# Kernel optimization log

Hardware: AMD Instinct MI355X
Metric: run time of the kernel (lower is better)

The kernel has to match this reference:

```python
import jax, jax.numpy as jnp
import numpy as np
from jax import lax

NUM_GROUPS = 16
EPS = 1e-5
POOL = 4
CLAMP_MIN, CLAMP_MAX = 0.0, 1.0


def setup_inputs() -> dict:
    key = jax.random.key(0)
    k = jax.random.split(key, 6)
    x = jax.random.normal(k[0], (128, 8, 128, 128), dtype=jnp.float32)
    conv_w = jax.random.normal(k[1], (64, 8, 3, 3), dtype=jnp.float32) * 0.1
    conv_b = jax.random.normal(k[2], (64,), dtype=jnp.float32) * 0.1
    gn_w = jnp.ones((64,), dtype=jnp.float32) + 0.1 * jax.random.normal(k[3], (64,), dtype=jnp.float32)
    gn_b = 0.1 * jax.random.normal(k[4], (64,), dtype=jnp.float32)
    scale = jnp.ones((64, 1, 1), dtype=jnp.float32) + 0.1 * jax.random.normal(k[5], (64, 1, 1), dtype=jnp.float32)
    return {"x": x, "conv_w": conv_w, "conv_b": conv_b, "gn_w": gn_w, "gn_b": gn_b, "scale": scale}


def reference(x, conv_w, conv_b, gn_w, gn_b, scale):
    # Conv2d: stride 1, no padding -> [N, 64, 126, 126]
    y = lax.conv_general_dilated(
        x, conv_w, window_strides=(1, 1), padding="VALID",
        dimension_numbers=("NCHW", "OIHW", "NCHW"))
    y = y + conv_b[None, :, None, None]

    # GroupNorm over (C/G, H, W) per (N, group), biased variance, eps=1e-5
    N, C, H, W = y.shape
    yg = y.reshape(N, NUM_GROUPS, -1)
    mean = jnp.mean(yg, axis=-1, keepdims=True)
    var = jnp.mean(jnp.square(yg - mean), axis=-1, keepdims=True)
    yn = ((yg - mean) * lax.rsqrt(var + EPS)).reshape(N, C, H, W)
    yn = yn * gn_w[None, :, None, None] + gn_b[None, :, None, None]

    # Per-channel scale (scale has shape [C,1,1])
    yn = yn * scale[None]

    # MaxPool2d(kernel=4, stride=4) -> [N, 64, 31, 31]
    yp = lax.reduce_window(yn, -jnp.inf, lax.max,
                           window_dimensions=(1, 1, POOL, POOL),
                           window_strides=(1, 1, POOL, POOL),
                           padding="VALID")

    # Clamp
    return jnp.clip(yp, CLAMP_MIN, CLAMP_MAX)
```

## Files before the change

kernel.cpp:

```cpp
#include <hip/hip_runtime.h>
#include <math.h>

#define N_IMG 128
#define IC 8
#define IH 128
#define IW 128
#define OC 64
#define OH 126
#define OW 126
#define NG 16
#define CPG 4
#define PH 31
#define PW 31
#define GN_EPS 1e-5f

__device__ __forceinline__ void conv4(const float* __restrict__ xb,
                                      const float* wlds_,
                                      int oh, int ow, bool edge,
                                      float acc[4][CPG]) {
#pragma unroll 1
    for (int ic = 0; ic < IC; ic++) {
        const float* xr = xb + ic * (IH * IW) + oh * IW + ow;
#pragma unroll
        for (int kh = 0; kh < 3; kh++) {
            const float* xrr = xr + kh * IW;
            float4 f4 = *(const float4*)xrr;
            float v0 = f4.x, v1 = f4.y, v2 = f4.z, v3 = f4.w;
            float v4 = 0.f, v5 = 0.f;
            if (!edge) {
                float2 f2 = *(const float2*)(xrr + 4);
                v4 = f2.x; v5 = f2.y;
            }
            const float* wk = wlds_ + (ic * 3 + kh) * 12;
            float wr[12];
#pragma unroll
            for (int t = 0; t < 12; t++) wr[t] = wk[t];
#pragma unroll
            for (int ch = 0; ch < CPG; ch++) {
                float w0 = wr[0 * 4 + ch];
                float w1 = wr[1 * 4 + ch];
                float w2 = wr[2 * 4 + ch];
                acc[0][ch] = fmaf(v0, w0, fmaf(v1, w1, fmaf(v2, w2, acc[0][ch])));
                acc[1][ch] = fmaf(v1, w0, fmaf(v2, w1, fmaf(v3, w2, acc[1][ch])));
                acc[2][ch] = fmaf(v2, w0, fmaf(v3, w1, fmaf(v4, w2, acc[2][ch])));
                acc[3][ch] = fmaf(v3, w0, fmaf(v4, w1, fmaf(v5, w2, acc[3][ch])));
            }
        }
    }
}

__launch_bounds__(256, 4)
__global__ void fused_conv_gn_pool_kernel(const float* __restrict__ x,
                                          const float* __restrict__ conv_w,
                                          const float* __restrict__ conv_b,
                                          const float* __restrict__ gn_w,
                                          const float* __restrict__ gn_b,
                                          const float* __restrict__ scale,
                                          float* __restrict__ out) {
    const int b = blockIdx.x;
    const int wid = ((b & 7) << 8) | (b >> 3);
    const int n = wid >> 4;
    const int g = wid & 15;
    const int tid = threadIdx.x;

    __shared__ float wlds[IC * 3 * 3 * CPG];
    __shared__ float red[8];
    __shared__ float stats[2];

    for (int t = tid; t < IC * 3 * 3 * CPG; t += 256) {
        int ch = t & 3;
        int r = t >> 2;
        int c = g * CPG + ch;
        float sg = (gn_w[c] * scale[c] >= 0.f) ? 1.f : -1.f;
        wlds[t] = conv_w[c * (IC * 9) + r] * sg;
    }
    float biasS[CPG], sgnf[CPG];
#pragma unroll
    for (int ch = 0; ch < CPG; ch++) {
        int c = g * CPG + ch;
        float sg = (gn_w[c] * scale[c] >= 0.f) ? 1.f : -1.f;
        sgnf[ch] = sg;
        biasS[ch] = conv_b[c] * sg;
    }
    __syncthreads();

    const float* xb = x + (size_t)n * (IC * IH * IW);

    float s_ch[CPG];
    float ss = 0.f;
#pragma unroll
    for (int ch = 0; ch < CPG; ch++) s_ch[ch] = 0.f;
    float pm[4][CPG];
#pragma unroll
    for (int ci = 0; ci < 4; ci++)
#pragma unroll
        for (int ch = 0; ch < CPG; ch++) pm[ci][ch] = -INFINITY;

#pragma unroll
    for (int ci = 0; ci < 4; ci++) {
        int cell = tid + ci * 256;
        if (cell < PH * PW) {
            int ph = cell / PW;
            int pw = cell - ph * PW;
            const float* xcell = xb + 4 * pw;
#pragma unroll
            for (int rp = 0; rp < 2; rp++) {
                const int r0 = 4 * ph + 2 * rp;
                float acc[2][4][CPG];
#pragma unroll
                for (int rr = 0; rr < 2; rr++)
#pragma unroll
                    for (int j = 0; j < 4; j++)
#pragma unroll
                        for (int ch = 0; ch < CPG; ch++) acc[rr][j][ch] = biasS[ch];

#pragma unroll 2
                for (int ic = 0; ic < IC; ic++) {
                    const float* xr = xcell + ic * (IH * IW) + r0 * IW;
                    float xv[4][6];
#pragma unroll
                    for (int rr = 0; rr < 4; rr++) {
                        float4 f4 = *(const float4*)(xr + rr * IW);
                        float2 f2 = *(const float2*)(xr + rr * IW + 4);
                        xv[rr][0] = f4.x; xv[rr][1] = f4.y;
                        xv[rr][2] = f4.z; xv[rr][3] = f4.w;
                        xv[rr][4] = f2.x; xv[rr][5] = f2.y;
                    }
                    const float* wk = wlds + ic * 36;
#pragma unroll
                    for (int kh = 0; kh < 3; kh++) {
                        float wr[12];
#pragma unroll
                        for (int t = 0; t < 12; t++) wr[t] = wk[kh * 12 + t];
#pragma unroll
                        for (int ch = 0; ch < CPG; ch++) {
                            float w0 = wr[0 * 4 + ch];
                            float w1 = wr[1 * 4 + ch];
                            float w2 = wr[2 * 4 + ch];
#pragma unroll
                            for (int j = 0; j < 4; j++) {
                                acc[0][j][ch] = fmaf(xv[kh][j],     w0,
                                                fmaf(xv[kh][j + 1], w1,
                                                fmaf(xv[kh][j + 2], w2, acc[0][j][ch])));
                                acc[1][j][ch] = fmaf(xv[kh + 1][j],     w0,
                                                fmaf(xv[kh + 1][j + 1], w1,
                                                fmaf(xv[kh + 1][j + 2], w2, acc[1][j][ch])));
                            }
                        }
                    }
                }
#pragma unroll
                for (int rr = 0; rr < 2; rr++)
#pragma unroll
                    for (int j = 0; j < 4; j++)
#pragma unroll
                        for (int ch = 0; ch < CPG; ch++) {
                            float v = acc[rr][j][ch];
                            s_ch[ch] += v;
                            ss = fmaf(v, v, ss);
                            pm[ci][ch] = fmaxf(pm[ci][ch], v);
                        }
            }
        }
    }

    if (tid < 124) {
        float acc[4][CPG];
#pragma unroll
        for (int j = 0; j < 4; j++)
#pragma unroll
            for (int ch = 0; ch < CPG; ch++) acc[j][ch] = biasS[ch];
        conv4(xb, wlds, tid, 124, true, acc);
#pragma unroll
        for (int j = 0; j < 2; j++)
#pragma unroll
            for (int ch = 0; ch < CPG; ch++) {
                float v = acc[j][ch];
                s_ch[ch] += v;
                ss = fmaf(v, v, ss);
            }
    } else if (tid >= 128 && tid < 192) {
        int idx = tid - 128;
        int oh = 124 + (idx >> 5);
        int q = idx & 31;
        bool edge = (q == 31);
        float acc[4][CPG];
#pragma unroll
        for (int j = 0; j < 4; j++)
#pragma unroll
            for (int ch = 0; ch < CPG; ch++) acc[j][ch] = biasS[ch];
        conv4(xb, wlds, oh, q * 4, edge, acc);
        int jmax = edge ? 2 : 4;
#pragma unroll
        for (int j = 0; j < 4; j++) {
            if (j < jmax) {
#pragma unroll
                for (int ch = 0; ch < CPG; ch++) {
                    float v = acc[j][ch];
                    s_ch[ch] += v;
                    ss = fmaf(v, v, ss);
                }
            }
        }
    }

    float s = sgnf[0] * s_ch[0] + sgnf[1] * s_ch[1]
            + sgnf[2] * s_ch[2] + sgnf[3] * s_ch[3];
#pragma unroll
    for (int off = 32; off > 0; off >>= 1) {
        s  += __shfl_down(s, off, 64);
        ss += __shfl_down(ss, off, 64);
    }
    int wave = tid >> 6;
    if ((tid & 63) == 0) { red[wave] = s; red[4 + wave] = ss; }
    __syncthreads();
    if (tid == 0) {
        float S  = red[0] + red[1] + red[2] + red[3];
        float SS = red[4] + red[5] + red[6] + red[7];
        const float inv_count = 1.f / (float)(CPG * OH * OW);
        float mean = S * inv_count;
        float var = SS * inv_count - mean * mean;
        if (var < 0.f) var = 0.f;
        stats[0] = mean;
        stats[1] = rsqrtf(var + GN_EPS);
    }
    __syncthreads();
    const float mean = stats[0];
    const float rstd = stats[1];

    float a2[CPG], b2[CPG];
#pragma unroll
    for (int ch = 0; ch < CPG; ch++) {
        int c = g * CPG + ch;
        float gw = gn_w[c], sc = scale[c];
        a2[ch] = rstd * fabsf(gw * sc);
        b2[ch] = (gn_b[c] - mean * rstd * gw) * sc;
    }

#pragma unroll
    for (int ci = 0; ci < 4; ci++) {
        int cell = tid + ci * 256;
        if (cell < PH * PW) {
            int ph = cell / PW;
            int pw = cell - ph * PW;
#pragma unroll
            for (int ch = 0; ch < CPG; ch++) {
                int c = g * CPG + ch;
                float v = fmaf(a2[ch], pm[ci][ch], b2[ch]);
                v = fminf(fmaxf(v, 0.f), 1.f);
                out[(((size_t)n * OC + c) * PH + ph) * PW + pw] = v;
            }
        }
    }
}

extern "C" void kernel_launch(void* const* d_in, const int* in_sizes, int n_in,
                              void* d_out, int out_size, void* d_ws, size_t ws_size,
                              hipStream_t stream) {
    const float* x      = (const float*)d_in[0];
    const float* conv_w = (const float*)d_in[1];
    const float* conv_b = (const float*)d_in[2];
    const float* gn_w   = (const float*)d_in[3];
    const float* gn_b   = (const float*)d_in[4];
    const float* scale  = (const float*)d_in[5];
    float* out = (float*)d_out;

    dim3 grid(N_IMG * NG);
    dim3 block(256);
    hipLaunchKernelGGL(fused_conv_gn_pool_kernel, grid, block, 0, stream,
                       x, conv_w, conv_b, gn_w, gn_b, scale, out);
}
```

Baseline: 349.1 us.

## Compute full 4x4 pool cell per pass to reuse input rows

Each thread now computes all four conv rows of a pool cell in a single pass, loading six input rows per channel instead of four rows twice, which cuts redundant global loads. The accumulator tile doubles to 4x4x4 registers, so launch bounds are relaxed from 4 to 3 blocks per SM and the cell and channel loops are no longer unrolled to keep register pressure under control. Sum-of-squares is split into per-channel accumulators to shorten the dependency chain. The trade-off is lower occupancy and possible register spills.

```diff
diff --git a/kernel.cpp b/kernel.cpp
--- a/kernel.cpp
+++ b/kernel.cpp
@@ -49,7 +49,7 @@
     }
 }
 
-__launch_bounds__(256, 4)
+__launch_bounds__(256, 3)
 __global__ void fused_conv_gn_pool_kernel(const float* __restrict__ x,
                                           const float* __restrict__ conv_w,
                                           const float* __restrict__ conv_b,
@@ -87,80 +87,79 @@
     const float* xb = x + (size_t)n * (IC * IH * IW);
 
     float s_ch[CPG];
-    float ss = 0.f;
-#pragma unroll
-    for (int ch = 0; ch < CPG; ch++) s_ch[ch] = 0.f;
+    float ss_ch[CPG];
+#pragma unroll
+    for (int ch = 0; ch < CPG; ch++) { s_ch[ch] = 0.f; ss_ch[ch] = 0.f; }
     float pm[4][CPG];
 #pragma unroll
     for (int ci = 0; ci < 4; ci++)
 #pragma unroll
         for (int ch = 0; ch < CPG; ch++) pm[ci][ch] = -INFINITY;
 
-#pragma unroll
+#pragma unroll 1
     for (int ci = 0; ci < 4; ci++) {
         int cell = tid + ci * 256;
         if (cell < PH * PW) {
             int ph = cell / PW;
             int pw = cell - ph * PW;
-            const float* xcell = xb + 4 * pw;
-#pragma unroll
-            for (int rp = 0; rp < 2; rp++) {
-                const int r0 = 4 * ph + 2 * rp;
-                float acc[2][4][CPG];
-#pragma unroll
-                for (int rr = 0; rr < 2; rr++)
-#pragma unroll
-                    for (int j = 0; j < 4; j++)
-#pragma unroll
-                        for (int ch = 0; ch < CPG; ch++) acc[rr][j][ch] = biasS[ch];
-
-#pragma unroll 2
-                for (int ic = 0; ic < IC; ic++) {
-                    const float* xr = xcell + ic * (IH * IW) + r0 * IW;
-                    float xv[4][6];
-#pragma unroll
-                    for (int rr = 0; rr < 4; rr++) {
-                        float4 f4 = *(const float4*)(xr + rr * IW);
-                        float2 f2 = *(const float2*)(xr + rr * IW + 4);
-                        xv[rr][0] = f4.x; xv[rr][1] = f4.y;
-                        xv[rr][2] = f4.z; xv[rr][3] = f4.w;
-                        xv[rr][4] = f2.x; xv[rr][5] = f2.y;
-                    }
-                    const float* wk = wlds + ic * 36;
-#pragma unroll
-                    for (int kh = 0; kh < 3; kh++) {
-                        float wr[12];
-#pragma unroll
-                        for (int t = 0; t < 12; t++) wr[t] = wk[kh * 12 + t];
-#pragma unroll
-                        for (int ch = 0; ch < CPG; ch++) {
-                            float w0 = wr[0 * 4 + ch];
-                            float w1 = wr[1 * 4 + ch];
-                            float w2 = wr[2 * 4 + ch];
+            const int r0 = 4 * ph;
+            const float* xcell = xb + r0 * IW + 4 * pw;
+
+            float acc[4][4][CPG];
+#pragma unroll
+            for (int rr = 0; rr < 4; rr++)
+#pragma unroll
+                for (int j = 0; j < 4; j++)
+#pragma unroll
+                    for (int ch = 0; ch < CPG; ch++) acc[rr][j][ch] = biasS[ch];
+
+#pragma unroll 1
+            for (int ic = 0; ic < IC; ic++) {
+                const float* xr = xcell + ic * (IH * IW);
+                float xv[6][6];
+#pragma unroll
+                for (int rr = 0; rr < 6; rr++) {
+                    float4 f4 = *(const float4*)(xr + rr * IW);
+                    float2 f2 = *(const float2*)(xr + rr * IW + 4);
+                    xv[rr][0] = f4.x; xv[rr][1] = f4.y;
+                    xv[rr][2] = f4.z; xv[rr][3] = f4.w;
+                    xv[rr][4] = f2.x; xv[rr][5] = f2.y;
+                }
+                const float* wk = wlds + ic * 36;
+#pragma unroll
+                for (int kh = 0; kh < 3; kh++) {
+                    float wr[12];
+#pragma unroll
+                    for (int t = 0; t < 12; t++) wr[t] = wk[kh * 12 + t];
+#pragma unroll
+                    for (int ch = 0; ch < CPG; ch++) {
+                        float w0 = wr[0 * 4 + ch];
+                        float w1 = wr[1 * 4 + ch];
+                        float w2 = wr[2 * 4 + ch];
+#pragma unroll
+                        for (int rr = 0; rr < 4; rr++) {
+                            const float* xrow = xv[rr + kh];
 #pragma unroll
                             for (int j = 0; j < 4; j++) {
-                                acc[0][j][ch] = fmaf(xv[kh][j],     w0,
-                                                fmaf(xv[kh][j + 1], w1,
-                                                fmaf(xv[kh][j + 2], w2, acc[0][j][ch])));
-                                acc[1][j][ch] = fmaf(xv[kh + 1][j],     w0,
-                                                fmaf(xv[kh + 1][j + 1], w1,
-                                                fmaf(xv[kh + 1][j + 2], w2, acc[1][j][ch])));
+                                acc[rr][j][ch] = fmaf(xrow[j],     w0,
+                                                 fmaf(xrow[j + 1], w1,
+                                                 fmaf(xrow[j + 2], w2, acc[rr][j][ch])));
                             }
                         }
                     }
                 }
-#pragma unroll
-                for (int rr = 0; rr < 2; rr++)
-#pragma unroll
-                    for (int j = 0; j < 4; j++)
-#pragma unroll
-                        for (int ch = 0; ch < CPG; ch++) {
-                            float v = acc[rr][j][ch];
-                            s_ch[ch] += v;
-                            ss = fmaf(v, v, ss);
-                            pm[ci][ch] = fmaxf(pm[ci][ch], v);
-                        }
-            }
+            }
+#pragma unroll
+            for (int rr = 0; rr < 4; rr++)
+#pragma unroll
+                for (int j = 0; j < 4; j++)
+#pragma unroll
+                    for (int ch = 0; ch < CPG; ch++) {
+                        float v = acc[rr][j][ch];
+                        s_ch[ch] += v;
+                        ss_ch[ch] = fmaf(v, v, ss_ch[ch]);
+                        pm[ci][ch] = fmaxf(pm[ci][ch], v);
+                    }
         }
     }
 
@@ -177,7 +176,7 @@
             for (int ch = 0; ch < CPG; ch++) {
                 float v = acc[j][ch];
                 s_ch[ch] += v;
-                ss = fmaf(v, v, ss);
+                ss_ch[ch] = fmaf(v, v, ss_ch[ch]);
             }
     } else if (tid >= 128 && tid < 192) {
         int idx = tid - 128;
@@ -198,7 +197,7 @@
                 for (int ch = 0; ch < CPG; ch++) {
                     float v = acc[j][ch];
                     s_ch[ch] += v;
-                    ss = fmaf(v, v, ss);
+                    ss_ch[ch] = fmaf(v, v, ss_ch[ch]);
                 }
             }
         }
@@ -206,6 +205,7 @@
 
     float s = sgnf[0] * s_ch[0] + sgnf[1] * s_ch[1]
             + sgnf[2] * s_ch[2] + sgnf[3] * s_ch[3];
+    float ss = ss_ch[0] + ss_ch[1] + ss_ch[2] + ss_ch[3];
 #pragma unroll
     for (int off = 32; off > 0; off >>= 1) {
         s  += __shfl_down(s, off, 64);
```

After: 324.3 us. -7.1%, faster.
